# Performance work log

Hardware: AMD Instinct MI355X
Metric: run time of the kernel (lower is better)

The kernel has to match this reference:

```python
import jax, jax.numpy as jnp
import numpy as np

IMAGE_W = 1024
IMAGE_H = 1024
STRIDES = (8, 16, 32, 64, 128)
TOP_N = 1000
MIN_SCORE = 0.05
NMS_THR = 0.6
MAX_DET = 100
NEG = -1e9  # sentinel for suppressed scores


def _positions(stride):
    # Faithful to repo: shifts_x indexed by feature_h, shifts_y by feature_w,
    # grid built [hf, wf, 2] = [shift_x_i, shift_y_j], then permute(1,0,2).
    hf, wf = IMAGE_H // stride, IMAGE_W // stride
    sx = (jnp.arange(hf, dtype=jnp.float32) + 0.5) * stride
    sy = (jnp.arange(wf, dtype=jnp.float32) + 0.5) * stride
    pos = jnp.stack(jnp.meshgrid(sx, sy, indexing='ij'), axis=-1)  # [hf, wf, 2]
    return jnp.transpose(pos, (1, 0, 2)).reshape(-1, 2)  # [hf*wf, 2]


def _filter_level(cls_h, reg_h, ctr_h, pos):
    B, C = cls_h.shape[0], cls_h.shape[-1]
    cls_h = jax.nn.sigmoid(cls_h).reshape(B, -1, C)
    reg_h = jnp.exp(reg_h).reshape(B, -1, 4)
    ctr_h = jax.nn.sigmoid(ctr_h).reshape(B, -1)
    scores = jnp.max(cls_h, axis=-1)
    classes = jnp.argmax(cls_h, axis=-1).astype(jnp.int32)
    scores = jnp.sqrt(scores * ctr_h)
    N = scores.shape[1]
    if N >= TOP_N:
        scores, idx = jax.lax.top_k(scores, TOP_N)  # sorted descending, like torch.topk
        classes = jnp.take_along_axis(classes, idx, axis=1)
        reg_h = jnp.take_along_axis(reg_h, idx[..., None], axis=1)
        posb = pos[idx]  # [B, TOP_N, 2]
    else:
        posb = jnp.broadcast_to(pos[None], (B, N, 2))
    return scores, classes, reg_h, posb


def _snap(reg, pos):
    # reg: [B, N, 4] (l,t,r,b), pos: [B, N, 2]
    b = jnp.concatenate([pos - reg[:, :, 0:2], pos + reg[:, :, 2:4]], axis=-1)
    b = b.astype(jnp.int32)  # torch .int() truncation
    b = jnp.stack([
        jnp.maximum(b[..., 0], 0),
        jnp.maximum(b[..., 1], 0),
        jnp.minimum(b[..., 2], IMAGE_W - 1),
        jnp.minimum(b[..., 3], IMAGE_H - 1),
    ], axis=-1)
    return b.astype(jnp.float32)


def _nms_image(scores, classes, boxes):
    # scores [N], classes [N] int32, boxes [N,4] float (already snapped to int grid)
    s = jnp.where(scores > MIN_SCORE, scores, NEG)
    x1, y1, x2, y2 = boxes[:, 0], boxes[:, 1], boxes[:, 2], boxes[:, 3]
    areas = (x2 - x1) * (y2 - y1)
    out_s = -jnp.ones((MAX_DET,), jnp.float32)
    out_c = -jnp.ones((MAX_DET,), jnp.float32)
    out_b = -jnp.ones((MAX_DET, 4), jnp.float32)

    def body(i, st):
        s, os_, oc, ob = st
        idx = jnp.argmax(s)            # highest remaining score -> sorted keep order
        ok = s[idx] > MIN_SCORE        # any un-suppressed valid candidate left?
        bb = boxes[idx]
        iw = jnp.clip(jnp.minimum(x2, bb[2]) - jnp.maximum(x1, bb[0]), 0.0)
        ih = jnp.clip(jnp.minimum(y2, bb[3]) - jnp.maximum(y1, bb[1]), 0.0)
        inter = iw * ih
        iou = inter / (areas + areas[idx] - inter + 1e-12)
        s = jnp.where((iou > NMS_THR) & ok, NEG, s)
        s = s.at[idx].set(NEG)
        os_ = os_.at[i].set(jnp.where(ok, scores[idx], -1.0))
        oc = oc.at[i].set(jnp.where(ok, classes[idx].astype(jnp.float32), -1.0))
        ob = ob.at[i].set(jnp.where(ok, bb, -jnp.ones((4,), jnp.float32)))
        return (s, os_, oc, ob)

    _, os_, oc, ob = jax.lax.fori_loop(0, MAX_DET, body, (s, out_s, out_c, out_b))
    return os_, oc, ob


def _decode(cls_heads, reg_heads, ctr_heads):
    sc_l, cl_l, rg_l, ps_l = [], [], [], []
    for c, r, t, st in zip(cls_heads, reg_heads, ctr_heads, STRIDES):
        sc, cl, rg, ps = _filter_level(c, r, t, _positions(st))
        sc_l.append(sc); cl_l.append(cl); rg_l.append(rg); ps_l.append(ps)
    scores = jnp.concatenate(sc_l, axis=1)
    classes = jnp.concatenate(cl_l, axis=1)
    regs = jnp.concatenate(rg_l, axis=1)
    poss = jnp.concatenate(ps_l, axis=1)
    boxes = _snap(regs, poss)
    return jax.vmap(_nms_image)(scores, classes, boxes)


def setup_inputs() -> dict:
    key = jax.random.key(0)
    ks = jax.random.split(key, 15)
    B, C = 8, 80
    sizes = [IMAGE_H // s for s in STRIDES]
    inp = {}
    for i, hw in enumerate(sizes):
        inp[f'cls{i}'] = jax.random.normal(ks[i], (B, hw, hw, C), dtype=jnp.float32)
        # +3 so exp(reg) gives realistic ~20px extents
        inp[f'reg{i}'] = jax.random.normal(ks[5 + i], (B, hw, hw, 4), dtype=jnp.float32) + 3.0
        inp[f'ctr{i}'] = jax.random.normal(ks[10 + i], (B, hw, hw, 1), dtype=jnp.float32)
    return inp


def reference(cls0, cls1, cls2, cls3, cls4,
              reg0, reg1, reg2, reg3, reg4,
              ctr0, ctr1, ctr2, ctr3, ctr4):
    cls_heads = [cls0, cls1, cls2, cls3, cls4]
    reg_heads = [reg0, reg1, reg2, reg3, reg4]
    ctr_heads = [ctr0, ctr1, ctr2, ctr3, ctr4]
    batch_scores, batch_classes, batch_boxes = _decode(cls_heads, reg_heads, ctr_heads)
    return batch_scores, batch_classes, batch_boxes
```

## Files before the change

### kernel.cpp

```cpp
#include <hip/hip_runtime.h>

#define NPOS 21824
#define MINS 0.05f
#define BT2  256
#define NW2  4
#define TFAST 0.85f
#define SEC  8
#define SCAP 2048
#define CAP  (SEC*SCAP)
#define SLCAP 3072
#define CSTRIDE 32

struct Ptrs { const float* cls[5]; const float* reg[5]; const float* ctr[5]; };

__device__ __forceinline__ float sigf(float x){ return 1.0f/(1.0f+expf(-x)); }

__device__ __forceinline__ void cstore_u32(unsigned* p, unsigned v){
    __hip_atomic_store(p, v, __ATOMIC_RELAXED, __HIP_MEMORY_SCOPE_AGENT);
}
__device__ __forceinline__ void cstore_i32(int* p, int v){
    __hip_atomic_store(p, v, __ATOMIC_RELAXED, __HIP_MEMORY_SCOPE_AGENT);
}
__device__ __forceinline__ void cstore_u64(unsigned long long* p, unsigned long long v){
    __hip_atomic_store(p, v, __ATOMIC_RELAXED, __HIP_MEMORY_SCOPE_AGENT);
}
__device__ __forceinline__ unsigned cload_u32(const unsigned* p){
    return __hip_atomic_load(p, __ATOMIC_RELAXED, __HIP_MEMORY_SCOPE_AGENT);
}
__device__ __forceinline__ int cload_i32(const int* p){
    return __hip_atomic_load(p, __ATOMIC_RELAXED, __HIP_MEMORY_SCOPE_AGENT);
}
__device__ __forceinline__ unsigned long long cload_u64(const unsigned long long* p){
    return __hip_atomic_load(p, __ATOMIC_RELAXED, __HIP_MEMORY_SCOPE_AGENT);
}

__device__ __forceinline__ unsigned long long mkkey(unsigned int b, int p){
    return ((unsigned long long)b << 16) | (unsigned)(65535 - p);
}

__device__ __forceinline__ float4 computeBox(const Ptrs& P, int img, int p){
    int base, lw, stride, lvl;
    if (p < 16384)      { lvl=0; base=0;     lw=7; stride=8;   }
    else if (p < 20480) { lvl=1; base=16384; lw=6; stride=16;  }
    else if (p < 21504) { lvl=2; base=20480; lw=5; stride=32;  }
    else if (p < 21760) { lvl=3; base=21504; lw=4; stride=64;  }
    else                { lvl=4; base=21760; lw=3; stride=128; }
    int pl = p - base;
    int h = pl >> lw, w = pl & ((1<<lw)-1);
    long long lidx = (long long)img*(1<<(2*lw)) + pl;
    float4 rg = ((const float4*)P.reg[lvl])[lidx];
    float x = (w + 0.5f)*(float)stride;
    float y = (h + 0.5f)*(float)stride;
    int ix1 = (int)(x - expf(rg.x));
    int iy1 = (int)(y - expf(rg.y));
    int ix2 = (int)(x + expf(rg.z));
    int iy2 = (int)(y + expf(rg.w));
    ix1 = max(ix1,0); iy1 = max(iy1,0);
    ix2 = min(ix2,1023); iy2 = min(iy2,1023);
    return make_float4((float)ix1,(float)iy1,(float)ix2,(float)iy2);
}

__device__ void suffix_pick(const int* hist, int* wsum, int K,
                            unsigned int prefBase, int shift,
                            unsigned int* shPref, int* shK, int tid)
{
    const int g = 2048 / BT2;
    int lo = tid*g, ls = 0;
#pragma unroll
    for (int q = 0; q < g; ++q) ls += hist[lo + q];
    int lane = tid & 63, wv = tid >> 6;
    int v = ls;
#pragma unroll
    for (int off = 1; off < 64; off <<= 1) {
        int o = __shfl_down(v, off);
        if (lane + off < 64) v += o;
    }
    if (lane == 0) wsum[wv] = v;
    __syncthreads();
    int add = 0;
    for (int q = wv + 1; q < NW2; ++q) add += wsum[q];
    int mine = v + add;
    int above = mine - ls;
    if (above < K && mine >= K) {
        int cum = above;
        for (int b = lo + g - 1; b >= lo; --b) {
            cum += hist[b];
            if (cum >= K) {
                *shPref = prefBase | ((unsigned)b << shift);
                *shK = K - (cum - hist[b]);
                break;
            }
        }
    }
    __syncthreads();
}

__global__ __launch_bounds__(BT2) void k_all(Ptrs P, float* scoreAll, int* clsAll,
                                             unsigned long long* list, int* secCnt,
                                             int* dSec, int* dImg, float* out)
{
    __shared__ __align__(16) unsigned long long slist[SLCAP];
    __shared__ int hist[2048];
    __shared__ unsigned long long sel[256];
    __shared__ unsigned long long eqKey[256];
    __shared__ int wsum[NW2];
    __shared__ int cntS[SEC], offS[SEC+1];
    __shared__ unsigned int shPref;
    __shared__ int shK, tick, eqn;
    __shared__ int shNaM, shNa, shTotal, shMaxS;
    __shared__ unsigned long long shLast;
    __shared__ int lcnt, lbase, lastFlag;

    unsigned long long* sorted = (unsigned long long*)((char*)slist + 0);
    float4* sBox  = (float4*)((char*)slist + 2048);
    float*  sCls  = (float*)((char*)slist + 6144);
    int*    accIdx= (int*)((char*)slist + 7168);
    float4* accBox= (float4*)((char*)slist + 7680);
    unsigned long long (*sRow)[4] =
        (unsigned long long (*)[4])((char*)slist + 9472);

    int tid = threadIdx.x;
    int img = blockIdx.y;
    int blk = blockIdx.x;
    int s   = blk & 7;
    int ssz = (s < 5) ? 43 : 42;

    {
        int posb = tid >> 2;
        int l    = tid & 3;
        int p    = blk*64 + posb;
        int lvl, base, lw;
        if (blk < 256)      { lvl=0; base=0;     lw=7; }
        else if (blk < 320) { lvl=1; base=16384; lw=6; }
        else if (blk < 336) { lvl=2; base=20480; lw=5; }
        else if (blk < 340) { lvl=3; base=21504; lw=4; }
        else                { lvl=4; base=21760; lw=3; }
        int pl = p - base;
        long long lidx = (long long)img*(1<<(2*lw)) + pl;

        if (tid == 0) lcnt = 0;
        __syncthreads();

        const float4* c4 = (const float4*)(P.cls[lvl] + lidx*80);
        float mx = -3.4e38f; int mi = 0;
#pragma unroll
        for (int j = 0; j < 5; ++j) {
            int k = j*4 + l;
            float4 v = c4[k];
            int cb = k*4;
            if (v.x > mx){mx=v.x; mi=cb;}
            if (v.y > mx){mx=v.y; mi=cb+1;}
            if (v.z > mx){mx=v.z; mi=cb+2;}
            if (v.w > mx){mx=v.w; mi=cb+3;}
        }
#pragma unroll
        for (int d = 1; d < 4; d <<= 1) {
            float omx = __shfl_xor(mx, d);
            int   omi = __shfl_xor(mi, d);
            if (omx > mx || (omx == mx && omi < mi)) { mx = omx; mi = omi; }
        }
        int myTicket = -1;
        unsigned long long myKey = 0;
        if (l == 0) {
            float ct = P.ctr[lvl][lidx];
            float sc = sqrtf(sigf(mx)*sigf(ct));
            int o = img*NPOS + p;
            cstore_u32((unsigned*)scoreAll + o, __float_as_uint(sc));
            cstore_i32(clsAll + o, mi);
            if (sc > TFAST) {
                myTicket = atomicAdd(&lcnt, 1);
                myKey = mkkey(__float_as_uint(sc), p);
            }
        }
        __syncthreads();
        if (tid == 0)
            lbase = lcnt ? __hip_atomic_fetch_add(&secCnt[(img*SEC+s)*CSTRIDE], lcnt,
                                __ATOMIC_RELAXED, __HIP_MEMORY_SCOPE_AGENT) : 0;
        __syncthreads();
        if (myTicket >= 0) {
            int t = lbase + myTicket;
            if (t < SCAP) cstore_u64(list + (long long)img*CAP + s*SCAP + t, myKey);
        }
    }

    __syncthreads();
    if (tid == 0) {
        lastFlag = 0;
        int t = __hip_atomic_fetch_add(&dSec[(img*SEC+s)*CSTRIDE], 1,
                                       __ATOMIC_RELAXED, __HIP_MEMORY_SCOPE_AGENT);
        if (t == ssz - 1) {
            int t2 = __hip_atomic_fetch_add(&dImg[img*CSTRIDE], 1,
                                       __ATOMIC_RELAXED, __HIP_MEMORY_SCOPE_AGENT);
            if (t2 == SEC - 1) lastFlag = 1;
        }
    }
    __syncthreads();
    if (!lastFlag) return;

    const unsigned int* gs = (const unsigned int*)scoreAll + (long long)img*NPOS;
    const int* gCls = clsAll + (long long)img*NPOS;
    const unsigned long long* gl = list + (long long)img*CAP;

    float* outS = out + img*100;
    float* outC = out + 800 + img*100;
    float* outB = out + 1600 + img*400;

    if (tid < SEC) cntS[tid] = cload_i32(&secCnt[(img*SEC+tid)*CSTRIDE]);
    if (tid == 0) { tick = 0; eqn = 0; }
    __syncthreads();
    if (tid == 0) {
        int o = 0, mx = 0;
        for (int q = 0; q < SEC; ++q) {
            offS[q] = o;
            int c = cntS[q];
            o += c; if (c > mx) mx = c;
        }
        offS[SEC] = o; shTotal = o; shMaxS = mx;
    }
    __syncthreads();
    int total = shTotal;
    bool fastPath = (total >= 256 && total <= SLCAP && shMaxS <= SCAP);

    if (fastPath) {
        for (int q = 0; q < SEC; ++q) {
            int c = cntS[q], o = offS[q];
            const unsigned long long* seg = gl + q*SCAP;
            for (int i = tid; i < c; i += BT2) slist[o + i] = cload_u64(seg + i);
        }
    }
    for (int i = tid; i < 2048; i += BT2) hist[i] = 0;
    __syncthreads();

    unsigned int kth; int need;
    if (fastPath) {
        for (int i = tid; i < total; i += BT2)
            atomicAdd(&hist[(unsigned)(slist[i] >> 35)], 1);
        __syncthreads();
        suffix_pick(hist, wsum, 256, 0u, 19, &shPref, &shK, tid);
        unsigned int pref = shPref; int K2 = shK;
        for (int i = tid; i < 2048; i += BT2) hist[i] = 0;
        __syncthreads();
        for (int i = tid; i < total; i += BT2) {
            unsigned long long k = slist[i];
            if ((unsigned)(k >> 35) == (pref >> 19))
                atomicAdd(&hist[(unsigned)(k >> 24) & 2047], 1);
        }
        __syncthreads();
        suffix_pick(hist, wsum, K2, pref, 8, &shPref, &shK, tid);
        kth = shPref >> 8; need = shK;
        for (int i = tid; i < total; i += BT2) {
            unsigned long long k = slist[i];
            unsigned int hb = (unsigned)(k >> 24);
            if (hb > kth)       { int t = atomicAdd(&tick, 1); sel[t] = k; }
            else if (hb == kth) { int t = atomicAdd(&eqn, 1); if (t < 256) eqKey[t] = k; }
        }
    } else {
        for (int i = tid; i < NPOS; i += BT2)
            atomicAdd(&hist[cload_u32(gs + i) >> 19], 1);
        __syncthreads();
        suffix_pick(hist, wsum, 256, 0u, 19, &shPref, &shK, tid);
        unsigned int pref = shPref; int K2 = shK;
        for (int i = tid; i < 2048; i += BT2) hist[i] = 0;
        __syncthreads();
        for (int i = tid; i < NPOS; i += BT2) {
            unsigned int b = cload_u32(gs + i);
            if ((b >> 19) == (pref >> 19)) atomicAdd(&hist[(b >> 8) & 2047], 1);
        }
        __syncthreads();
        suffix_pick(hist, wsum, K2, pref, 8, &shPref, &shK, tid);
        kth = shPref >> 8; need = shK;
        for (int i = tid; i < NPOS; i += BT2) {
            unsigned int b = cload_u32(gs + i), hb = b >> 8;
            if (hb > kth)       { int t = atomicAdd(&tick, 1); sel[t] = mkkey(b, i); }
            else if (hb == kth) { int t = atomicAdd(&eqn, 1); if (t < 256) eqKey[t] = mkkey(b, i); }
        }
    }
    __syncthreads();
    int m = eqn, nG = tick;
    if (m <= 256) {
        for (int q = tid; q < m; q += BT2) {
            unsigned long long kq = eqKey[q];
            int r = 0;
            for (int j = 0; j < m; ++j) r += (eqKey[j] > kq);
            if (r < need) sel[nG + r] = kq;
        }
    } else if (tid == 0) {
        unsigned long long last = ~0ULL;
        for (int c = 0; c < need; ++c) {
            unsigned long long best = 0;
            if (fastPath) {
                for (int i = 0; i < total; ++i) {
                    unsigned long long k2 = slist[i];
                    if ((unsigned)(k2 >> 24) == kth && k2 < last && k2 > best) best = k2;
                }
            } else {
                for (int i = 0; i < NPOS; ++i) {
                    unsigned int b = cload_u32(gs + i);
                    if ((b >> 8) == kth) {
                        unsigned long long k2 = mkkey(b, i);
                        if (k2 < last && k2 > best) best = k2;
                    }
                }
            }
            sel[nG + c] = best; last = best;
        }
    }
    __syncthreads();

    {
        unsigned long long k = sel[tid];
        int r = 0;
        for (int j = 0; j < 256; ++j) r += (sel[j] > k);
        sorted[r] = k;
    }
    __syncthreads();
    {
        int p = 65535 - (int)(sorted[tid] & 0xFFFF);
        sBox[tid] = computeBox(P, img, p);
        sCls[tid] = (float)cload_i32(gCls + p);
    }

    float myScore = __uint_as_float((unsigned int)(sorted[tid] >> 16));
    int nValid = __syncthreads_count(myScore > MINS ? 1 : 0);

    {
        float4 bi = sBox[tid];
        float  ai = (bi.z-bi.x)*(bi.w-bi.y);
#pragma unroll
        for (int qq = 0; qq < 4; ++qq) {
            unsigned long long mv = 0;
#pragma unroll 8
            for (int jj = 0; jj < 64; ++jj) {
                int j = qq*64 + jj;
                float4 bj = sBox[j];
                float aj = (bj.z-bj.x)*(bj.w-bj.y);
                float iw = fmaxf(fminf(bj.z,bi.z)-fmaxf(bj.x,bi.x),0.f);
                float ih = fmaxf(fminf(bj.w,bi.w)-fmaxf(bj.y,bi.y),0.f);
                float in_ = iw*ih;
                bool s2 = (j > tid) && (in_/(aj+ai-in_+1e-12f) > 0.6f);
                mv |= ((unsigned long long)s2) << jj;
            }
            sRow[tid][qq] = mv;
        }
    }
    __syncthreads();

    if (tid == 0) {
        int na = 0;
        unsigned long long r0=0, r1=0, r2=0, r3=0;
#define FCOS_WBLK(RW, IB)                                                  \
        {                                                                  \
            int hi = nValid < ((IB)+1)*64 ? nValid : ((IB)+1)*64;          \
            for (int i = (IB)*64; i < hi && na < 100; ++i) {               \
                if ((RW >> (i - (IB)*64)) & 1ull) continue;                \
                accIdx[na++] = i;                                          \
                const ulonglong2* rp = (const ulonglong2*)sRow[i];         \
                ulonglong2 ra = rp[0], rb = rp[1];                         \
                r0 |= ra.x; r1 |= ra.y; r2 |= rb.x; r3 |= rb.y;            \
            }                                                              \
        }
        FCOS_WBLK(r0,0) FCOS_WBLK(r1,1) FCOS_WBLK(r2,2) FCOS_WBLK(r3,3)
#undef FCOS_WBLK
        shNaM = na; shNa = na;
    }
    __syncthreads();

    int naM = shNaM;
    if (naM < 100 && nValid == 256) {
        if (tid < naM) accBox[tid] = sBox[accIdx[tid]];
        if (tid == 0) shLast = sorted[255];
        __syncthreads();
        while (true) {
            if (shNa >= 100) break;
            unsigned long long last = shLast;
            unsigned long long bk = 0;
            for (int i = tid; i < NPOS; i += BT2) {
                unsigned long long k2 = mkkey(cload_u32(gs + i), i);
                if (k2 < last && k2 > bk) bk = k2;
            }
#pragma unroll
            for (int off = 32; off > 0; off >>= 1) {
                unsigned long long o = __shfl_down(bk, off);
                if (o > bk) bk = o;
            }
            int lane = tid & 63, wv = tid >> 6;
            if (lane == 0) eqKey[wv] = bk;
            __syncthreads();
            if (tid == 0) {
                unsigned long long best = 0;
                for (int q = 0; q < NW2; ++q) if (eqKey[q] > best) best = eqKey[q];
                shLast = best;
            }
            __syncthreads();
            unsigned long long ck = shLast;
            if (ck == 0ULL) break;
            float sc = __uint_as_float((unsigned int)(ck >> 16));
            if (!(sc > MINS)) break;
            int p = 65535 - (int)(ck & 0xFFFF);
            float4 bb = computeBox(P, img, p);
            float ba = (bb.z-bb.x)*(bb.w-bb.y);
            int na = shNa;
            bool mySup = false;
            if (tid < na) {
                float4 ab = accBox[tid];
                float aa = (ab.z-ab.x)*(ab.w-ab.y);
                float iw = fmaxf(fminf(bb.z,ab.z)-fmaxf(bb.x,ab.x),0.f);
                float ih = fmaxf(fminf(bb.w,ab.w)-fmaxf(bb.y,ab.y),0.f);
                float in_ = iw*ih;
                mySup = in_/(ba+aa-in_+1e-12f) > 0.6f;
            }
            int supCnt = __syncthreads_count(mySup);
            if (supCnt == 0) {
                if (tid == 0) {
                    int na2 = shNa;
                    outS[na2] = sc;
                    outC[na2] = (float)cload_i32(gCls + p);
                    outB[4*na2+0]=bb.x; outB[4*na2+1]=bb.y;
                    outB[4*na2+2]=bb.z; outB[4*na2+3]=bb.w;
                    accBox[na2] = bb;
                    shNa = na2 + 1;
                }
            }
            __syncthreads();
        }
    }
    __syncthreads();

    {
        int naM2 = shNaM, naT = shNa;
        if (tid < 100) {
            if (tid < naM2) {
                int r = accIdx[tid];
                unsigned long long k = sorted[r];
                float4 b = sBox[r];
                outS[tid] = __uint_as_float((unsigned int)(k >> 16));
                outC[tid] = sCls[r];
                outB[4*tid+0]=b.x; outB[4*tid+1]=b.y;
                outB[4*tid+2]=b.z; outB[4*tid+3]=b.w;
            } else if (tid >= naT) {
                outS[tid] = -1.f; outC[tid] = -1.f;
                outB[4*tid+0]=-1.f; outB[4*tid+1]=-1.f;
                outB[4*tid+2]=-1.f; outB[4*tid+3]=-1.f;
            }
        }
    }
}

extern "C" void kernel_launch(void* const* d_in, const int* in_sizes, int n_in,
                              void* d_out, int out_size, void* d_ws, size_t ws_size,
                              hipStream_t stream) {
    Ptrs P;
    bool interleaved = (in_sizes[1] == 8 * 128 * 128 * 4);
    for (int i = 0; i < 5; ++i) {
        if (interleaved) {
            P.cls[i] = (const float*)d_in[3*i];
            P.reg[i] = (const float*)d_in[3*i + 1];
            P.ctr[i] = (const float*)d_in[3*i + 2];
        } else {
            P.cls[i] = (const float*)d_in[i];
            P.reg[i] = (const float*)d_in[5 + i];
            P.ctr[i] = (const float*)d_in[10 + i];
        }
    }

    char* wbase = (char*)d_ws;
    size_t off = 0;
    auto alloc = [&](size_t bytes) -> void* {
        void* r = wbase + off;
        off += (bytes + 255) & ~(size_t)255;
        return r;
    };
    float*              scoreAll = (float*)alloc((size_t)8 * NPOS * 4);
    int*                clsAll   = (int*)alloc((size_t)8 * NPOS * 4);
    unsigned long long* list     = (unsigned long long*)alloc((size_t)8 * CAP * 8);
    int*                secCnt   = (int*)alloc((size_t)8 * SEC * CSTRIDE * 4);
    int*                dSec     = (int*)alloc((size_t)8 * SEC * CSTRIDE * 4);
    int*                dImg     = (int*)alloc((size_t)8 * CSTRIDE * 4);

    hipMemsetAsync(secCnt, 0,
                   (size_t)(8*SEC*CSTRIDE + 8*SEC*CSTRIDE + 8*CSTRIDE) * 4, stream);

    dim3 gA(341, 8);
    k_all<<<gA, BT2, 0, stream>>>(P, scoreAll, clsAll, list, secCnt, dSec, dImg,
                                  (float*)d_out);
}
```

Baseline: 171.2 us.

## Drop shared candidate staging buffer and stream keys from global in selection

```diff
diff --git a/kernel.cpp b/kernel.cpp
--- a/kernel.cpp
+++ b/kernel.cpp
@@ -8,7 +8,6 @@
 #define SEC  8
 #define SCAP 2048
 #define CAP  (SEC*SCAP)
-#define SLCAP 3072
 #define CSTRIDE 32
 
 struct Ptrs { const float* cls[5]; const float* reg[5]; const float* ctr[5]; };
@@ -99,10 +98,10 @@
                                              unsigned long long* list, int* secCnt,
                                              int* dSec, int* dImg, float* out)
 {
-    __shared__ __align__(16) unsigned long long slist[SLCAP];
-    __shared__ int hist[2048];
-    __shared__ unsigned long long sel[256];
-    __shared__ unsigned long long eqKey[256];
+    __shared__ __align__(16) char pool[8192 + 2048 + 2112];
+    __shared__ float4 sBox[256];
+    __shared__ float  sCls[256];
+    __shared__ unsigned long long redBuf[NW2];
     __shared__ int wsum[NW2];
     __shared__ int cntS[SEC], offS[SEC+1];
     __shared__ unsigned int shPref;
@@ -111,13 +110,13 @@
     __shared__ unsigned long long shLast;
     __shared__ int lcnt, lbase, lastFlag;
 
-    unsigned long long* sorted = (unsigned long long*)((char*)slist + 0);
-    float4* sBox  = (float4*)((char*)slist + 2048);
-    float*  sCls  = (float*)((char*)slist + 6144);
-    int*    accIdx= (int*)((char*)slist + 7168);
-    float4* accBox= (float4*)((char*)slist + 7680);
-    unsigned long long (*sRow)[4] =
-        (unsigned long long (*)[4])((char*)slist + 9472);
+    int* hist = (int*)pool;
+    unsigned long long (*sRow)[4] = (unsigned long long (*)[4])pool;
+    unsigned long long* eqKey  = (unsigned long long*)(pool + 8192);
+    unsigned long long* sorted = (unsigned long long*)(pool + 8192);
+    unsigned long long* sel    = (unsigned long long*)(pool + 10240);
+    int*    accIdx = (int*)(pool + 10240);
+    float4* accBox = (float4*)(pool + 10240 + 512);
 
     int tid = threadIdx.x;
     int img = blockIdx.y;
@@ -207,6 +206,7 @@
 
     if (tid < SEC) cntS[tid] = cload_i32(&secCnt[(img*SEC+tid)*CSTRIDE]);
     if (tid == 0) { tick = 0; eqn = 0; }
+    for (int i = tid; i < 2048; i += BT2) hist[i] = 0;
     __syncthreads();
     if (tid == 0) {
         int o = 0, mx = 0;
@@ -219,40 +219,42 @@
     }
     __syncthreads();
     int total = shTotal;
-    bool fastPath = (total >= 256 && total <= SLCAP && shMaxS <= SCAP);
-
+    bool fastPath = (total >= 256 && shMaxS <= SCAP);
+
+    unsigned int kth; int need;
     if (fastPath) {
         for (int q = 0; q < SEC; ++q) {
-            int c = cntS[q], o = offS[q];
+            int c = cntS[q];
             const unsigned long long* seg = gl + q*SCAP;
-            for (int i = tid; i < c; i += BT2) slist[o + i] = cload_u64(seg + i);
-        }
-    }
-    for (int i = tid; i < 2048; i += BT2) hist[i] = 0;
-    __syncthreads();
-
-    unsigned int kth; int need;
-    if (fastPath) {
-        for (int i = tid; i < total; i += BT2)
-            atomicAdd(&hist[(unsigned)(slist[i] >> 35)], 1);
+            for (int i = tid; i < c; i += BT2)
+                atomicAdd(&hist[(unsigned)(cload_u64(seg + i) >> 35)], 1);
+        }
         __syncthreads();
         suffix_pick(hist, wsum, 256, 0u, 19, &shPref, &shK, tid);
         unsigned int pref = shPref; int K2 = shK;
         for (int i = tid; i < 2048; i += BT2) hist[i] = 0;
         __syncthreads();
-        for (int i = tid; i < total; i += BT2) {
-            unsigned long long k = slist[i];
-            if ((unsigned)(k >> 35) == (pref >> 19))
-                atomicAdd(&hist[(unsigned)(k >> 24) & 2047], 1);
+        for (int q = 0; q < SEC; ++q) {
+            int c = cntS[q];
+            const unsigned long long* seg = gl + q*SCAP;
+            for (int i = tid; i < c; i += BT2) {
+                unsigned long long k = cload_u64(seg + i);
+                if ((unsigned)(k >> 35) == (pref >> 19))
+                    atomicAdd(&hist[(unsigned)(k >> 24) & 2047], 1);
+            }
         }
         __syncthreads();
         suffix_pick(hist, wsum, K2, pref, 8, &shPref, &shK, tid);
         kth = shPref >> 8; need = shK;
-        for (int i = tid; i < total; i += BT2) {
-            unsigned long long k = slist[i];
-            unsigned int hb = (unsigned)(k >> 24);
-            if (hb > kth)       { int t = atomicAdd(&tick, 1); sel[t] = k; }
-            else if (hb == kth) { int t = atomicAdd(&eqn, 1); if (t < 256) eqKey[t] = k; }
+        for (int q = 0; q < SEC; ++q) {
+            int c = cntS[q];
+            const unsigned long long* seg = gl + q*SCAP;
+            for (int i = tid; i < c; i += BT2) {
+                unsigned long long k = cload_u64(seg + i);
+                unsigned int hb = (unsigned)(k >> 24);
+                if (hb > kth)       { int t = atomicAdd(&tick, 1); sel[t] = k; }
+                else if (hb == kth) { int t = atomicAdd(&eqn, 1); if (t < 256) eqKey[t] = k; }
+            }
         }
     } else {
         for (int i = tid; i < NPOS; i += BT2)
@@ -289,9 +291,13 @@
         for (int c = 0; c < need; ++c) {
             unsigned long long best = 0;
             if (fastPath) {
-                for (int i = 0; i < total; ++i) {
-                    unsigned long long k2 = slist[i];
-                    if ((unsigned)(k2 >> 24) == kth && k2 < last && k2 > best) best = k2;
+                for (int q = 0; q < SEC; ++q) {
+                    int cq = cntS[q];
+                    const unsigned long long* seg = gl + q*SCAP;
+                    for (int i = 0; i < cq; ++i) {
+                        unsigned long long k2 = cload_u64(seg + i);
+                        if ((unsigned)(k2 >> 24) == kth && k2 < last && k2 > best) best = k2;
+                    }
                 }
             } else {
                 for (int i = 0; i < NPOS; ++i) {
@@ -384,11 +390,11 @@
                 if (o > bk) bk = o;
             }
             int lane = tid & 63, wv = tid >> 6;
-            if (lane == 0) eqKey[wv] = bk;
+            if (lane == 0) redBuf[wv] = bk;
             __syncthreads();
             if (tid == 0) {
                 unsigned long long best = 0;
-                for (int q = 0; q < NW2; ++q) if (eqKey[q] > best) best = eqKey[q];
+                for (int q = 0; q < NW2; ++q) if (redBuf[q] > best) best = redBuf[q];
                 shLast = best;
             }
             __syncthreads();
```

Result: slower. 180.0 us (+5.1%).
